# Performance work log

Hardware: AMD Instinct MI355X
Metric: run time of the kernel (lower is better)

The kernel has to match this reference:

```python
import jax, jax.numpy as jnp
import numpy as np

NEG = -1e30  # finite stand-in for -inf (keeps gradients NaN-free)
BLANK = 0    # PyTorch nn.CTCLoss default blank index


def setup_inputs() -> dict:
    key = jax.random.key(0)
    k1, k2, k3 = jax.random.split(key, 3)
    T, B, C, S = 512, 1024, 63, 25
    # model emits log-probabilities (log_softmax output), as nn.CTCLoss expects
    log_probs = jax.nn.log_softmax(jax.random.normal(k1, (T, B, C), jnp.float32), axis=-1)
    targets = jax.random.randint(k2, (B, S), 1, C, dtype=jnp.int32)        # labels in [1, C)
    target_lengths = jax.random.randint(k3, (B,), 10, S + 1, dtype=jnp.int32)
    return {"log_probs": log_probs, "targets": targets, "target_lengths": target_lengths}


def _ctc_loss(log_probs, targets, target_lengths):
    # log_probs: [T, B, C]; targets: [B, S] padded; target_lengths: [B]
    T, B, C = log_probs.shape
    S = targets.shape[1]
    L = 2 * S + 1  # extended target: blank-interleaved

    ext = jnp.zeros((B, L), targets.dtype).at[:, 1::2].set(targets)  # [B, L]
    prev2 = jnp.concatenate([jnp.full((B, 2), -1, ext.dtype), ext[:, :-2]], axis=1)
    skip = (ext != BLANK) & (ext != prev2)  # allow alpha[s-2] transition

    # t = 0 init: only positions 0 (blank) and 1 (first label) reachable
    lp0 = log_probs[0]  # [B, C]
    alpha0 = jnp.full((B, L), NEG, log_probs.dtype)
    alpha0 = alpha0.at[:, 0].set(lp0[:, BLANK])
    alpha0 = alpha0.at[:, 1].set(jnp.take_along_axis(lp0, ext[:, 1:2], axis=1)[:, 0])

    def step(alpha, lp_t):  # alpha: [B, L], lp_t: [B, C]
        lp_ext = jnp.take_along_axis(lp_t, ext, axis=1)  # [B, L]
        a1 = alpha
        a2 = jnp.pad(alpha[:, :-1], ((0, 0), (1, 0)), constant_values=NEG)
        a3 = jnp.where(skip, jnp.pad(alpha[:, :-2], ((0, 0), (2, 0)), constant_values=NEG), NEG)
        m = jnp.maximum(jnp.maximum(a1, a2), a3)
        new = m + jnp.log(jnp.exp(a1 - m) + jnp.exp(a2 - m) + jnp.exp(a3 - m)) + lp_ext
        return new, None

    alpha_T, _ = jax.lax.scan(step, alpha0, log_probs[1:])

    # log-likelihood = logaddexp of the last two reachable positions (2*len, 2*len-1)
    idx = jnp.stack([2 * target_lengths - 1, 2 * target_lengths], axis=1)  # [B, 2]
    a_fin = jnp.take_along_axis(alpha_T, idx, axis=1)
    ll = jnp.logaddexp(a_fin[:, 0], a_fin[:, 1])
    nll = -ll
    nll = jnp.where(nll > 0.5e30, 0.0, nll)  # zero_infinity=True
    # PyTorch reduction='mean': divide each loss by its target length, then batch mean
    return jnp.mean(nll / jnp.maximum(target_lengths, 1).astype(nll.dtype))


def reference(log_probs, targets, target_lengths):
    return _ctc_loss(log_probs, targets, target_lengths)
```

## Files before the change

kernel.cpp:

```cpp
#include <hip/hip_runtime.h>


#define TT 512
#define BB 1024
#define CC 63
#define SS 25
#define D  32
#define LN2F 0.69314718055994531f

__device__ __forceinline__ float shr1f(float x, float fill) {
  return __int_as_float(__builtin_amdgcn_update_dpp(
      __float_as_int(fill), __float_as_int(x), 0x138, 0xF, 0xF, false));
}
__device__ __forceinline__ int shr1i(int x, int fill) {
  return __builtin_amdgcn_update_dpp(fill, x, 0x138, 0xF, 0xF, false);
}

__global__ __launch_bounds__(256) void ctc_alpha_kernel(
    const float* __restrict__ logp,
    const int* __restrict__ targets,
    const int* __restrict__ tlen,
    float* __restrict__ loss) {
  const int lane = threadIdx.x & 63;
  const int b = (blockIdx.x << 2) + (threadIdx.x >> 6);
  const int* tg = targets + b * SS;
  const int len = tlen[b];

  int e = 0;
  float skf = 0.0f;
  if (lane & 1) {
    const int i = lane >> 1;
    if (i < SS) {
      e = tg[i];
      skf = (e != 0 && (i == 0 || e != tg[i - 1])) ? 1.0f : 0.0f;
    }
  }

  const unsigned SB = (unsigned)(BB * CC) * 4u;
  unsigned off = (unsigned)(b * CC + e) * 4u;
  const char* base = (const char*)logp;
#define LDF(O) (*(const float*)(base + (O)))

  float A = (lane <= 1) ? __expf(LDF(off)) : 0.0f;
  int M2 = 0;
  float F1 = 1.0f, F2s = skf;

  float pf[D];
  unsigned offp = off + SB;
#pragma unroll
  for (int j = 0; j < D; ++j) { pf[j] = LDF(offp); offp += SB; }

#define RENORM() {                                              \
    int e2 = (int)(__float_as_uint(A) >> 23) - 127;             \
    A = ldexpf(A, -e2);                              \
    int m2n = M2 + e2;                                          \
    int m2a = shr1i(m2n, 0);                                    \
    M2 = (A == 0.0f) ? m2a : m2n;     \
    int s1 = shr1i(M2, 0);                                      \
    int s2 = shr1i(s1, 0);                                      \
    int d1 = s1 - M2, d2 = s2 - M2;                             \
    d1 = d1 < -126 ? -126 : (d1 > 126 ? 126 : d1);              \
    d2 = d2 < -126 ? -126 : (d2 > 126 ? 126 : d2);              \
    F1 = ldexpf(1.0f, d1);                      \
    F2s = skf * ldexpf(1.0f, d2);                               \
  }

#define STEP(J, PF) {                                           \
    const float P = __expf(pf[(J)]);                            \
    const float a2 = shr1f(A, 0.0f);                            \
    const float a3 = shr1f(a2, 0.0f);                           \
    A = P * fmaf(F2s, a3, fmaf(F1, a2, A));                     \
    if (PF) { pf[(J)] = LDF(offp); offp += SB; }                \
    if (((J) & 15) == 15) RENORM()                              \
  }

  for (int blk = 0; blk < 14; ++blk) {
#pragma unroll
    for (int j = 0; j < D; ++j) STEP(j, true)
  }
#pragma unroll
  for (int j = 0; j < D; ++j) STEP(j, j < 31)
#pragma unroll
  for (int j = 0; j < 31; ++j) STEP(j, false)

  const int ia = 2 * len - 1, ib = 2 * len;
  const float aA = __shfl(A, ia), aB = __shfl(A, ib);
  const int mA = __shfl(M2, ia), mB = __shfl(M2, ib);
  if (lane == 0) {
    const float la = (float)mA * LN2F + logf(aA);
    const float lb = (float)mB * LN2F + logf(aB);
    const float m = fmaxf(la, lb);
    const float ll = m + logf(expf(la - m) + expf(lb - m));
    float nll = -ll;
    if (!(nll <= 0.5e30f)) nll = 0.0f;
    const int dl = len > 1 ? len : 1;
    loss[b] = nll / (float)dl;
  }
}

__global__ __launch_bounds__(256) void ctc_reduce_kernel(
    const float* __restrict__ loss, float* __restrict__ out) {
  float s = 0.f;
  for (int i = threadIdx.x; i < BB; i += 256) s += loss[i];
#pragma unroll
  for (int off = 32; off; off >>= 1) s += __shfl_down(s, off);
  __shared__ float sm[4];
  if ((threadIdx.x & 63) == 0) sm[threadIdx.x >> 6] = s;
  __syncthreads();
  if (threadIdx.x == 0) out[0] = (sm[0] + sm[1] + sm[2] + sm[3]) / (float)BB;
}

extern "C" void kernel_launch(void* const* d_in, const int* in_sizes, int n_in,
                              void* d_out, int out_size, void* d_ws, size_t ws_size,
                              hipStream_t stream) {
  const float* logp  = (const float*)d_in[0];
  const int* targets = (const int*)d_in[1];
  const int* tlen    = (const int*)d_in[2];
  float* out  = (float*)d_out;
  float* loss = (float*)d_ws;
  hipLaunchKernelGGL(ctc_alpha_kernel, dim3(BB / 4), dim3(256), 0, stream,
                     logp, targets, tlen, loss);
  hipLaunchKernelGGL(ctc_reduce_kernel, dim3(1), dim3(256), 0, stream, loss, out);
}
```

Baseline: 33.66 us.

## Split CTC recursion into concurrent forward and backward half-sequence wavefronts

Result: faster. 32.92 us (-2.2%).

```diff
diff --git a/kernel.cpp b/kernel.cpp
--- a/kernel.cpp
+++ b/kernel.cpp
@@ -6,6 +6,7 @@
 #define CC 63
 #define SS 25
 #define D  32
+#define NEGV (-1e30f)
 #define LN2F 0.69314718055994531f
 
 __device__ __forceinline__ float shr1f(float x, float fill) {
@@ -15,86 +16,148 @@
 __device__ __forceinline__ int shr1i(int x, int fill) {
   return __builtin_amdgcn_update_dpp(fill, x, 0x138, 0xF, 0xF, false);
 }
+__device__ __forceinline__ float shl1f(float x, float fill) {
+  return __int_as_float(__builtin_amdgcn_update_dpp(
+      __float_as_int(fill), __float_as_int(x), 0x130, 0xF, 0xF, false));
+}
+__device__ __forceinline__ int shl1i(int x, int fill) {
+  return __builtin_amdgcn_update_dpp(fill, x, 0x130, 0xF, 0xF, false);
+}
+__device__ __forceinline__ int iclamp126(int d) {
+  return d < -126 ? -126 : (d > 126 ? 126 : d);
+}
 
-__global__ __launch_bounds__(256) void ctc_alpha_kernel(
+__global__ __launch_bounds__(256) void ctc_fb_kernel(
     const float* __restrict__ logp,
     const int* __restrict__ targets,
     const int* __restrict__ tlen,
     float* __restrict__ loss) {
   const int lane = threadIdx.x & 63;
-  const int b = (blockIdx.x << 2) + (threadIdx.x >> 6);
+  const int wid = threadIdx.x >> 6;
+  const int pairIdx = wid >> 1;
+  const int bwd = wid & 1;
+  const int b = (blockIdx.x << 1) + pairIdx;
   const int* tg = targets + b * SS;
   const int len = tlen[b];
 
   int e = 0;
   float skf = 0.0f;
+  float skf2 = 0.0f;
   if (lane & 1) {
     const int i = lane >> 1;
     if (i < SS) {
       e = tg[i];
-      skf = (e != 0 && (i == 0 || e != tg[i - 1])) ? 1.0f : 0.0f;
+      skf = (i == 0 || e != tg[i - 1]) ? 1.0f : 0.0f;
+      if (i + 1 < SS) skf2 = (tg[i + 1] != tg[i]) ? 1.0f : 0.0f;
     }
   }
 
   const unsigned SB = (unsigned)(BB * CC) * 4u;
-  unsigned off = (unsigned)(b * CC + e) * 4u;
   const char* base = (const char*)logp;
+  const unsigned off0 = (unsigned)(b * CC + e) * 4u;
 #define LDF(O) (*(const float*)(base + (O)))
 
-  float A = (lane <= 1) ? __expf(LDF(off)) : 0.0f;
+  __shared__ float la_s[2][64];
+
+  float A, F1, F2m;
   int M2 = 0;
-  float F1 = 1.0f, F2s = skf;
+  float pf[D];
+  unsigned offp;
 
-  float pf[D];
-  unsigned offp = off + SB;
+  if (!bwd) {
+    A = (lane <= 1) ? __expf(LDF(off0)) : 0.0f;
+    F1 = 1.0f; F2m = skf;
+    offp = off0 + SB;
 #pragma unroll
-  for (int j = 0; j < D; ++j) { pf[j] = LDF(offp); offp += SB; }
+    for (int j = 0; j < D; ++j) { pf[j] = LDF(offp); offp += SB; }
 
-#define RENORM() {                                              \
-    int e2 = (int)(__float_as_uint(A) >> 23) - 127;             \
-    A = ldexpf(A, -e2);                              \
-    int m2n = M2 + e2;                                          \
-    int m2a = shr1i(m2n, 0);                                    \
-    M2 = (A == 0.0f) ? m2a : m2n;     \
-    int s1 = shr1i(M2, 0);                                      \
-    int s2 = shr1i(s1, 0);                                      \
-    int d1 = s1 - M2, d2 = s2 - M2;                             \
-    d1 = d1 < -126 ? -126 : (d1 > 126 ? 126 : d1);              \
-    d2 = d2 < -126 ? -126 : (d2 > 126 ? 126 : d2);              \
-    F1 = ldexpf(1.0f, d1);                      \
-    F2s = skf * ldexpf(1.0f, d2);                               \
+#define RENF() {                                               \
+    int e2 = (int)(__float_as_uint(A) >> 23) - 127;            \
+    A = ldexpf(A, -e2);                                        \
+    int m2n = M2 + e2;                                         \
+    int m2a = shr1i(m2n, 0);                                   \
+    M2 = (A == 0.0f) ? m2a : m2n;                              \
+    int s1 = shr1i(M2, 0), s2 = shr1i(s1, 0);                  \
+    F1 = ldexpf(1.0f, iclamp126(s1 - M2));                     \
+    F2m = skf * ldexpf(1.0f, iclamp126(s2 - M2));              \
+  }
+#define STEPF(J, PFLAG) {                                      \
+    const float P = __expf(pf[(J)]);                           \
+    const float c1 = P * F1, c2 = P * F2m;                     \
+    const float a2 = shr1f(A, 0.0f);                           \
+    const float pa = P * A;                                    \
+    const float a3 = shr1f(a2, 0.0f);                          \
+    A = fmaf(c2, a3, fmaf(c1, a2, pa));                        \
+    if (PFLAG) { pf[(J)] = LDF(offp); offp += SB; }            \
+    if (((J) & 15) == 15) RENF()                               \
   }
 
-#define STEP(J, PF) {                                           \
-    const float P = __expf(pf[(J)]);                            \
-    const float a2 = shr1f(A, 0.0f);                            \
-    const float a3 = shr1f(a2, 0.0f);                           \
-    A = P * fmaf(F2s, a3, fmaf(F1, a2, A));                     \
-    if (PF) { pf[(J)] = LDF(offp); offp += SB; }                \
-    if (((J) & 15) == 15) RENORM()                              \
+    for (int blk = 0; blk < 6; ++blk) {
+#pragma unroll
+      for (int j = 0; j < D; ++j) STEPF(j, true)
+    }
+#pragma unroll
+    for (int j = 0; j < D; ++j) STEPF(j, j < 31)
+#pragma unroll
+    for (int j = 0; j < 31; ++j) STEPF(j, false)
+
+    la_s[pairIdx][lane] = fmaxf((float)M2 * LN2F + logf(A), NEGV);
+  } else {
+    A = (lane == 2 * len - 1 || lane == 2 * len) ? 1.0f : 0.0f;
+    F1 = 1.0f; F2m = skf2;
+    offp = 511u * SB + off0;
+#pragma unroll
+    for (int j = 0; j < D; ++j) { pf[j] = LDF(offp); offp -= SB; }
+
+#define RENB() {                                               \
+    int e2 = (int)(__float_as_uint(A) >> 23) - 127;            \
+    A = ldexpf(A, -e2);                                        \
+    int m2n = M2 + e2;                                         \
+    int m2a = shl1i(m2n, 0);                                   \
+    M2 = (A == 0.0f) ? m2a : m2n;                              \
+    int s1 = shl1i(M2, 0), s2 = shl1i(s1, 0);                  \
+    F1 = ldexpf(1.0f, iclamp126(s1 - M2));                     \
+    F2m = skf2 * ldexpf(1.0f, iclamp126(s2 - M2));             \
+  }
+#define STEPB(J, PFLAG) {                                      \
+    const float P = __expf(pf[(J)]);                           \
+    const float P1 = shl1f(P, 0.0f);                           \
+    const float P2 = shl1f(P1, 0.0f);                          \
+    const float c1 = F1 * P1, c2 = F2m * P2;                   \
+    const float a1 = shl1f(A, 0.0f);                           \
+    const float pa = P * A;                                    \
+    const float a2 = shl1f(a1, 0.0f);                          \
+    A = fmaf(c2, a2, fmaf(c1, a1, pa));                        \
+    if (PFLAG) { pf[(J)] = LDF(offp); offp -= SB; }            \
+    if (((J) & 15) == 15) RENB()                               \
   }
 
-  for (int blk = 0; blk < 14; ++blk) {
+    for (int blk = 0; blk < 7; ++blk) {
 #pragma unroll
-    for (int j = 0; j < D; ++j) STEP(j, true)
+      for (int j = 0; j < D; ++j) STEPB(j, true)
+    }
+#pragma unroll
+    for (int j = 0; j < D; ++j) STEPB(j, false)
   }
+
+  __syncthreads();
+
+  if (bwd) {
+    const float lb = fmaxf((float)M2 * LN2F + logf(A), NEGV);
+    float v = (lane <= 50) ? la_s[pairIdx][lane] + lb : -2e30f;
+    float m = v;
 #pragma unroll
-  for (int j = 0; j < D; ++j) STEP(j, j < 31)
+    for (int o = 32; o; o >>= 1) m = fmaxf(m, __shfl_xor(m, o));
+    float s = __expf(v - m);
 #pragma unroll
-  for (int j = 0; j < 31; ++j) STEP(j, false)
-
-  const int ia = 2 * len - 1, ib = 2 * len;
-  const float aA = __shfl(A, ia), aB = __shfl(A, ib);
-  const int mA = __shfl(M2, ia), mB = __shfl(M2, ib);
-  if (lane == 0) {
-    const float la = (float)mA * LN2F + logf(aA);
-    const float lb = (float)mB * LN2F + logf(aB);
-    const float m = fmaxf(la, lb);
-    const float ll = m + logf(expf(la - m) + expf(lb - m));
-    float nll = -ll;
-    if (!(nll <= 0.5e30f)) nll = 0.0f;
-    const int dl = len > 1 ? len : 1;
-    loss[b] = nll / (float)dl;
+    for (int o = 32; o; o >>= 1) s += __shfl_xor(s, o);
+    if (lane == 0) {
+      const float ll = m + logf(s);
+      float nll = -ll;
+      if (!(nll <= 0.5e30f)) nll = 0.0f;
+      const int dl = len > 1 ? len : 1;
+      loss[b] = nll / (float)dl;
+    }
   }
 }
 
@@ -118,7 +181,7 @@
   const int* tlen    = (const int*)d_in[2];
   float* out  = (float*)d_out;
   float* loss = (float*)d_ws;
-  hipLaunchKernelGGL(ctc_alpha_kernel, dim3(BB / 4), dim3(256), 0, stream,
+  hipLaunchKernelGGL(ctc_fb_kernel, dim3(BB / 2), dim3(256), 0, stream,
                      logp, targets, tlen, loss);
   hipLaunchKernelGGL(ctc_reduce_kernel, dim3(1), dim3(256), 0, stream, loss, out);
 }
```
